# Kernel tuning notes

Measured on AMD Instinct MI355X. Metric: run time of the kernel, lower is better.

## Reference

```python
import jax, jax.numpy as jnp
import numpy as np

PRUNE_N = 2  # entries zeroed per group
PRUNE_M = 4  # group size along feature dim


def _prune_2of4(x_flat):
    # x_flat: [N, D]; zero out the PRUNE_N smallest-|.| entries in every
    # contiguous group of PRUNE_M columns (matches torch topk(largest=False)
    # + scatter mask semantics, deterministic sort-order tie-breaking).
    N, D = x_flat.shape
    g = x_flat.reshape(N, D // PRUNE_M, PRUNE_M)           # [N, G, 4]
    a = jnp.abs(g)
    order = jnp.argsort(a, axis=-1)                         # ascending |.|
    rank = jnp.argsort(order, axis=-1)                      # rank of each slot
    keep = rank >= PRUNE_N                                  # keep 2 largest
    return jnp.where(keep, g, jnp.zeros_like(g)).reshape(N, D)


def setup_inputs() -> dict:
    key = jax.random.key(0)
    k1, k2 = jax.random.split(key)
    B, S, D_IN, D_OUT = 2, 4096, 4096, 4096
    x = jax.random.normal(k1, (B, S, D_IN), dtype=jnp.float32)
    weight = jax.random.normal(k2, (D_OUT, D_IN), dtype=jnp.float32) * 0.02
    return {"x": x, "weight": weight}


def reference(x, weight):
    B, S, D = x.shape
    x_flat = x.reshape(B * S, D)
    x_sp = _prune_2of4(x_flat)                              # [B*S, D]
    out = x_sp @ weight.T                                   # [B*S, D_out]
    return out
```

## Files before the change

### kernel.cpp

```cpp
#include <hip/hip_runtime.h>
#include <hip/hip_bf16.h>

typedef float f32x4 __attribute__((ext_vector_type(4)));
typedef __bf16 bf16x8 __attribute__((ext_vector_type(8)));
typedef unsigned short ushort_t;
typedef ushort_t u16x8 __attribute__((ext_vector_type(8)));

__device__ inline ushort_t f2bf_rne(float f) {
  unsigned u = __builtin_bit_cast(unsigned, f);
  unsigned r = (u + 0x7fffu + ((u >> 16) & 1u)) >> 16;
  return (ushort_t)r;
}

__global__ void prune_cast_kernel(const float* __restrict__ x,
                                  ushort_t* __restrict__ xsp, long n8) {
  long i = (long)blockIdx.x * blockDim.x + threadIdx.x;
  if (i >= n8) return;
  const float4* p = reinterpret_cast<const float4*>(x);
  float4 g0 = p[2 * i];
  float4 g1 = p[2 * i + 1];
  float v[8] = {g0.x, g0.y, g0.z, g0.w, g1.x, g1.y, g1.z, g1.w};
  u16x8 o;
#pragma unroll
  for (int g = 0; g < 2; ++g) {
    float a[4];
#pragma unroll
    for (int j = 0; j < 4; ++j) a[j] = fabsf(v[g * 4 + j]);
#pragma unroll
    for (int j = 0; j < 4; ++j) {
      int rank = 0;
#pragma unroll
      for (int k = 0; k < 4; ++k) {
        if (k == j) continue;
        rank += (a[k] < a[j]) || (a[k] == a[j] && k < j);
      }
      o[g * 4 + j] = (rank >= 2) ? f2bf_rne(v[g * 4 + j]) : (ushort_t)0;
    }
  }
  reinterpret_cast<u16x8*>(xsp)[i] = o;
}

__global__ void cast_bf16_kernel(const float* __restrict__ w,
                                 ushort_t* __restrict__ wb, long n8) {
  long i = (long)blockIdx.x * blockDim.x + threadIdx.x;
  if (i >= n8) return;
  const float4* p = reinterpret_cast<const float4*>(w);
  float4 g0 = p[2 * i];
  float4 g1 = p[2 * i + 1];
  u16x8 o;
  o[0] = f2bf_rne(g0.x); o[1] = f2bf_rne(g0.y);
  o[2] = f2bf_rne(g0.z); o[3] = f2bf_rne(g0.w);
  o[4] = f2bf_rne(g1.x); o[5] = f2bf_rne(g1.y);
  o[6] = f2bf_rne(g1.z); o[7] = f2bf_rne(g1.w);
  reinterpret_cast<u16x8*>(wb)[i] = o;
}

#define BARM()                              \
  asm volatile("" ::: "memory");            \
  __builtin_amdgcn_s_barrier();             \
  asm volatile("" ::: "memory");
#define WAIT_VM4() asm volatile("s_waitcnt vmcnt(4)" ::: "memory")
#define WAIT_VM0() asm volatile("s_waitcnt vmcnt(0)" ::: "memory")

#define STAGE_A(t1, h, par)                                                    \
  {                                                                            \
    const ushort_t* g0 =                                                       \
        A + (a_row0 + (h) * 128 + srow) * (long)Kd + (t1) * 64 + scol;         \
    const ushort_t* g1 =                                                       \
        A + (a_row0 + (h) * 128 + srow + 8) * (long)Kd + (t1) * 64 + scol;     \
    ushort_t* l0 = &ldsA[((par) * 2 + (h)) * 8192 + w * 1024];                 \
    __builtin_amdgcn_global_load_lds(                                          \
        (const __attribute__((address_space(1))) void*)g0,                     \
        (__attribute__((address_space(3))) void*)l0, 16, 0, 0);                \
    __builtin_amdgcn_global_load_lds(                                          \
        (const __attribute__((address_space(1))) void*)g1,                     \
        (__attribute__((address_space(3))) void*)(l0 + 512), 16, 0, 0);        \
  }

#define STAGE_B(t1, h, par)                                                    \
  {                                                                            \
    const ushort_t* g0 =                                                       \
        B + (b_row0 + (h) * 128 + srow) * (long)Kd + (t1) * 64 + scol;         \
    const ushort_t* g1 =                                                       \
        B + (b_row0 + (h) * 128 + srow + 8) * (long)Kd + (t1) * 64 + scol;     \
    ushort_t* l0 = &ldsB[((par) * 2 + (h)) * 8192 + w * 1024];                 \
    __builtin_amdgcn_global_load_lds(                                          \
        (const __attribute__((address_space(1))) void*)g0,                     \
        (__attribute__((address_space(3))) void*)l0, 16, 0, 0);                \
    __builtin_amdgcn_global_load_lds(                                          \
        (const __attribute__((address_space(1))) void*)g1,                     \
        (__attribute__((address_space(3))) void*)(l0 + 512), 16, 0, 0);        \
  }

#define LDA_FRAG(dst, par, mi, s)                                              \
  dst = *reinterpret_cast<const bf16x8*>(                                      \
      reinterpret_cast<const char*>(ldsA) + ((par) * 2 + wr) * 16384 +         \
      (mi) * 2048 + ((s) ? roff1 : roff0));

#define LDB_FRAG(dst, par, ni, s)                                              \
  dst = *reinterpret_cast<const bf16x8*>(                                      \
      reinterpret_cast<const char*>(ldsB) + ((par) * 2 + (wc >> 1)) * 16384 +  \
      (wc & 1) * 8192 + (ni) * 2048 + ((s) ? roff1 : roff0));

#define MFMA_Q(MH, NH)                                                         \
  __builtin_amdgcn_s_setprio(1);                                               \
  _Pragma("unroll") for (int s = 0; s < 2; ++s)                                \
  _Pragma("unroll") for (int mi = 0; mi < 4; ++mi)                             \
  _Pragma("unroll") for (int ni = 0; ni < 2; ++ni)                             \
      acc[(MH) * 4 + mi][(NH) * 2 + ni] =                                      \
          __builtin_amdgcn_mfma_f32_16x16x32_bf16(                             \
              af[mi][s], bfr[(NH) * 2 + ni][s],                                \
              acc[(MH) * 4 + mi][(NH) * 2 + ni], 0, 0, 0);                     \
  __builtin_amdgcn_s_setprio(0);

#define KTILE(t, PAR)                                                          \
  {                                                                            \
    const int tA = ((t) + 1 < NT) ? (t) + 1 : NT - 1;                          \
    const int tB = ((t) + 2 < NT) ? (t) + 2 : NT - 1;                          \
            \
    _Pragma("unroll") for (int mi = 0; mi < 4; ++mi)                           \
    _Pragma("unroll") for (int s = 0; s < 2; ++s)                              \
        LDA_FRAG(af[mi][s], PAR, mi, s)                                        \
    _Pragma("unroll") for (int ni = 0; ni < 4; ++ni)                           \
    _Pragma("unroll") for (int s = 0; s < 2; ++s)                              \
        LDB_FRAG(bfr[ni][s], PAR, ni, s)                                       \
    STAGE_A(tA, 0, (PAR) ^ 1)                                                  \
    STAGE_A(tA, 1, (PAR) ^ 1)                                                  \
    MFMA_Q(0, 0)                                                               \
    MFMA_Q(0, 1)                                                               \
    _Pragma("unroll") for (int mi = 0; mi < 4; ++mi)                           \
    _Pragma("unroll") for (int s = 0; s < 2; ++s)                              \
        LDA_FRAG(af[mi][s], PAR, 4 + mi, s)                                    \
    MFMA_Q(1, 1)                                                               \
                     \
    BARM()                                                                     \
    STAGE_B(tB, 0, PAR)                                                        \
    STAGE_B(tB, 1, PAR)                                                        \
    MFMA_Q(1, 0)                                                               \
    WAIT_VM4();                                                                \
    BARM()                                                                     \
  }

__global__ __launch_bounds__(512, 1) void gemm256_kernel(
    const ushort_t* __restrict__ A,
    const ushort_t* __restrict__ B,
    float* __restrict__ C,
    int M, int N, int Kd) {
  __shared__ ushort_t ldsA[4 * 8192];
  __shared__ ushort_t ldsB[4 * 8192];

  const int tid = threadIdx.x;
  const int lane = tid & 63;
  const int w = tid >> 6;
  const int wr = w >> 2;
  const int wc = w & 3;

  const int b = blockIdx.x;
  const int wg = (b & 7) * (gridDim.x >> 3) + (b >> 3);
  const int nbn = N / 256;
  const int bm = wg / nbn, bn = wg % nbn;
  const long a_row0 = (long)bm * 256;
  const long b_row0 = (long)bn * 256;
  const int NT = Kd / 64;

  const int srow = w * 16 + (lane >> 3);
  const int scol = (((lane & 7) ^ ((lane >> 3) & 7)) << 3);

  const int rl = lane & 15;
  const int q = lane >> 4;
  const int roff0 = rl * 128 + (((q) ^ (rl & 7)) << 4);
  const int roff1 = rl * 128 + (((q | 4) ^ (rl & 7)) << 4);

  f32x4 acc[8][4];
#pragma unroll
  for (int i = 0; i < 8; ++i)
#pragma unroll
    for (int j = 0; j < 4; ++j) acc[i][j] = f32x4{0.f, 0.f, 0.f, 0.f};

  bf16x8 af[4][2];
  bf16x8 bfr[4][2];

  STAGE_A(0, 0, 0)
  STAGE_A(0, 1, 0)
  STAGE_B(0, 0, 0)
  STAGE_B(0, 1, 0)
  STAGE_B(1, 0, 1)
  STAGE_B(1, 1, 1)
  WAIT_VM4();
  BARM()

  for (int t = 0; t < NT; t += 2) {
    KTILE(t, 0)
    KTILE(t + 1, 1)
  }
  WAIT_VM0();

  const int orow = (lane >> 4) * 4;
  const int ocol = lane & 15;
#pragma unroll
  for (int mi = 0; mi < 8; ++mi)
#pragma unroll
    for (int ni = 0; ni < 4; ++ni) {
      const long r0 = a_row0 + wr * 128 + mi * 16 + orow;
      const long c0 = b_row0 + wc * 64 + ni * 16 + ocol;
#pragma unroll
      for (int r = 0; r < 4; ++r) C[(r0 + r) * N + c0] = acc[mi][ni][r];
    }
}

extern "C" void kernel_launch(void* const* d_in, const int* in_sizes, int n_in,
                              void* d_out, int out_size, void* d_ws,
                              size_t ws_size, hipStream_t stream) {
  const float* x = (const float*)d_in[0];
  const float* w = (const float*)d_in[1];
  float* out = (float*)d_out;

  const int K = 4096;
  const long M = (long)in_sizes[0] / K;
  const int N = in_sizes[1] / K;

  ushort_t* xsp = (ushort_t*)d_ws;
  ushort_t* wb = xsp + (long)M * K;

  const long n8x = M * K / 8;
  prune_cast_kernel<<<(int)((n8x + 255) / 256), 256, 0, stream>>>(x, xsp, n8x);

  const long n8w = (long)N * K / 8;
  cast_bf16_kernel<<<(int)((n8w + 255) / 256), 256, 0, stream>>>(w, wb, n8w);

  const int nwg = (int)(M / 256) * (N / 256);
  gemm256_kernel<<<nwg, 512, 0, stream>>>(xsp, wb, out, (int)M, N, K);
}
```

Baseline: 267.4 us.

## Switch GEMM inner loop from 16x16x32 to 32x32x16 bf16 MFMA

```diff
diff --git a/kernel.cpp b/kernel.cpp
--- a/kernel.cpp
+++ b/kernel.cpp
@@ -2,6 +2,7 @@
 #include <hip/hip_bf16.h>
 
 typedef float f32x4 __attribute__((ext_vector_type(4)));
+typedef float f32x16 __attribute__((ext_vector_type(16)));
 typedef __bf16 bf16x8 __attribute__((ext_vector_type(8)));
 typedef unsigned short ushort_t;
 typedef ushort_t u16x8 __attribute__((ext_vector_type(8)));
@@ -92,52 +93,57 @@
         (__attribute__((address_space(3))) void*)(l0 + 512), 16, 0, 0);        \
   }
 
-#define LDA_FRAG(dst, par, mi, s)                                              \
+#define LDA_FRAG(dst, par, mi, ks)                                             \
   dst = *reinterpret_cast<const bf16x8*>(                                      \
       reinterpret_cast<const char*>(ldsA) + ((par) * 2 + wr) * 16384 +         \
-      (mi) * 2048 + ((s) ? roff1 : roff0));
-
-#define LDB_FRAG(dst, par, ni, s)                                              \
+      (mi) * 4096 + rowb + koff[ks]);
+
+#define LDB_FRAG(dst, par, ni, ks)                                             \
   dst = *reinterpret_cast<const bf16x8*>(                                      \
       reinterpret_cast<const char*>(ldsB) + ((par) * 2 + (wc >> 1)) * 16384 +  \
-      (wc & 1) * 8192 + (ni) * 2048 + ((s) ? roff1 : roff0));
-
-#define MFMA_Q(MH, NH)                                                         \
+      (wc & 1) * 8192 + (ni) * 4096 + rowb + koff[ks]);
+
+#define MFMA_H0()                                                              \
   __builtin_amdgcn_s_setprio(1);                                               \
-  _Pragma("unroll") for (int s = 0; s < 2; ++s)                                \
-  _Pragma("unroll") for (int mi = 0; mi < 4; ++mi)                             \
+  _Pragma("unroll") for (int ks = 0; ks < 4; ++ks)                             \
+  _Pragma("unroll") for (int mi2 = 0; mi2 < 2; ++mi2)                          \
   _Pragma("unroll") for (int ni = 0; ni < 2; ++ni)                             \
-      acc[(MH) * 4 + mi][(NH) * 2 + ni] =                                      \
-          __builtin_amdgcn_mfma_f32_16x16x32_bf16(                             \
-              af[mi][s], bfr[(NH) * 2 + ni][s],                                \
-              acc[(MH) * 4 + mi][(NH) * 2 + ni], 0, 0, 0);                     \
+      acc[mi2][ni] = __builtin_amdgcn_mfma_f32_32x32x16_bf16(                  \
+          af[mi2][ks], bfr[ni][ks], acc[mi2][ni], 0, 0, 0);                    \
+  __builtin_amdgcn_s_setprio(0);
+
+#define MFMA_Q1(NH)                                                            \
+  __builtin_amdgcn_s_setprio(1);                                               \
+  _Pragma("unroll") for (int ks = 0; ks < 4; ++ks)                             \
+  _Pragma("unroll") for (int mi2 = 0; mi2 < 2; ++mi2)                          \
+      acc[2 + mi2][NH] = __builtin_amdgcn_mfma_f32_32x32x16_bf16(              \
+          af[mi2][ks], bfr[NH][ks], acc[2 + mi2][NH], 0, 0, 0);                \
   __builtin_amdgcn_s_setprio(0);
 
 #define KTILE(t, PAR)                                                          \
   {                                                                            \
     const int tA = ((t) + 1 < NT) ? (t) + 1 : NT - 1;                          \
     const int tB = ((t) + 2 < NT) ? (t) + 2 : NT - 1;                          \
-            \
-    _Pragma("unroll") for (int mi = 0; mi < 4; ++mi)                           \
-    _Pragma("unroll") for (int s = 0; s < 2; ++s)                              \
-        LDA_FRAG(af[mi][s], PAR, mi, s)                                        \
-    _Pragma("unroll") for (int ni = 0; ni < 4; ++ni)                           \
-    _Pragma("unroll") for (int s = 0; s < 2; ++s)                              \
-        LDB_FRAG(bfr[ni][s], PAR, ni, s)                                       \
+                \
+    _Pragma("unroll") for (int mi2 = 0; mi2 < 2; ++mi2)                        \
+    _Pragma("unroll") for (int ks = 0; ks < 4; ++ks)                           \
+        LDA_FRAG(af[mi2][ks], PAR, mi2, ks)                                    \
+    _Pragma("unroll") for (int ni = 0; ni < 2; ++ni)                           \
+    _Pragma("unroll") for (int ks = 0; ks < 4; ++ks)                           \
+        LDB_FRAG(bfr[ni][ks], PAR, ni, ks)                                     \
     STAGE_A(tA, 0, (PAR) ^ 1)                                                  \
     STAGE_A(tA, 1, (PAR) ^ 1)                                                  \
-    MFMA_Q(0, 0)                                                               \
-    MFMA_Q(0, 1)                                                               \
-    _Pragma("unroll") for (int mi = 0; mi < 4; ++mi)                           \
-    _Pragma("unroll") for (int s = 0; s < 2; ++s)                              \
-        LDA_FRAG(af[mi][s], PAR, 4 + mi, s)                                    \
-    MFMA_Q(1, 1)                                                               \
-                     \
+    MFMA_H0()                                                                  \
+    _Pragma("unroll") for (int mi2 = 0; mi2 < 2; ++mi2)                        \
+    _Pragma("unroll") for (int ks = 0; ks < 4; ++ks)                           \
+        LDA_FRAG(af[mi2][ks], PAR, 2 + mi2, ks)                                \
+    MFMA_Q1(1)                                                                 \
+            \
     BARM()                                                                     \
     STAGE_B(tB, 0, PAR)                                                        \
     STAGE_B(tB, 1, PAR)                                                        \
-    MFMA_Q(1, 0)                                                               \
-    WAIT_VM4();                                                                \
+    MFMA_Q1(0)                                                                 \
+    if ((t) + 2 < NT) { WAIT_VM4(); } else { WAIT_VM0(); }                     \
     BARM()                                                                     \
   }
 
@@ -166,19 +172,24 @@
   const int srow = w * 16 + (lane >> 3);
   const int scol = (((lane & 7) ^ ((lane >> 3) & 7)) << 3);
 
-  const int rl = lane & 15;
-  const int q = lane >> 4;
-  const int roff0 = rl * 128 + (((q) ^ (rl & 7)) << 4);
-  const int roff1 = rl * 128 + (((q | 4) ^ (rl & 7)) << 4);
-
-  f32x4 acc[8][4];
-#pragma unroll
-  for (int i = 0; i < 8; ++i)
-#pragma unroll
-    for (int j = 0; j < 4; ++j) acc[i][j] = f32x4{0.f, 0.f, 0.f, 0.f};
-
-  bf16x8 af[4][2];
-  bf16x8 bfr[4][2];
+  const int rl32 = lane & 31;
+  const int q32 = lane >> 5;
+  const int rowb = rl32 * 128;
+  const int rx = rl32 & 7;
+  int koff[4];
+#pragma unroll
+  for (int ks = 0; ks < 4; ++ks) koff[ks] = ((ks * 2 + q32) ^ rx) << 4;
+
+  f32x16 acc[4][2];
+#pragma unroll
+  for (int i = 0; i < 4; ++i)
+#pragma unroll
+    for (int j = 0; j < 2; ++j)
+#pragma unroll
+      for (int r = 0; r < 16; ++r) acc[i][j][r] = 0.f;
+
+  bf16x8 af[2][4];
+  bf16x8 bfr[2][4];
 
   STAGE_A(0, 0, 0)
   STAGE_A(0, 1, 0)
@@ -193,18 +204,18 @@
     KTILE(t, 0)
     KTILE(t + 1, 1)
   }
-  WAIT_VM0();
-
-  const int orow = (lane >> 4) * 4;
-  const int ocol = lane & 15;
-#pragma unroll
-  for (int mi = 0; mi < 8; ++mi)
-#pragma unroll
-    for (int ni = 0; ni < 4; ++ni) {
-      const long r0 = a_row0 + wr * 128 + mi * 16 + orow;
-      const long c0 = b_row0 + wc * 64 + ni * 16 + ocol;
-#pragma unroll
-      for (int r = 0; r < 4; ++r) C[(r0 + r) * N + c0] = acc[mi][ni][r];
+
+#pragma unroll
+  for (int mi = 0; mi < 4; ++mi)
+#pragma unroll
+    for (int ni = 0; ni < 2; ++ni) {
+      const long c0 = b_row0 + wc * 64 + ni * 32 + rl32;
+      const long r0 = a_row0 + wr * 128 + mi * 32 + q32 * 4;
+#pragma unroll
+      for (int r = 0; r < 16; ++r) {
+        const long row = r0 + (r & 3) + 8 * (r >> 2);
+        C[row * N + c0] = acc[mi][ni][r];
+      }
     }
 }
 
```

Result: slower. 306.2 us (+14.5%).
